# Kernel tuning notes

Measured on AMD Instinct MI355X. Metric: run time of the kernel, lower is better.

## Reference

```python
import jax, jax.numpy as jnp
import numpy as np

B, N, C, H = 8, 4096, 768, 8
EPS = 1e-12  # F.normalize eps


def setup_inputs() -> dict:
    key = jax.random.key(0)
    k1, k2, k3, k4 = jax.random.split(key, 4)
    x = jax.random.normal(k1, (B, N, C), dtype=jnp.float32)
    Wqkv = jax.random.normal(k2, (C, 3 * C), dtype=jnp.float32) * (1.0 / np.sqrt(C))
    temperature = jnp.ones((H, 1, 1), dtype=jnp.float32)
    Wproj = jax.random.normal(k3, (C, C), dtype=jnp.float32) * (1.0 / np.sqrt(C))
    bproj = jax.random.normal(k4, (C,), dtype=jnp.float32) * 0.01
    return {"x": x, "Wqkv": Wqkv, "temperature": temperature, "Wproj": Wproj, "bproj": bproj}


def _l2norm(t):
    # F.normalize(dim=-1): t / max(||t||_2, eps)
    n = jnp.sqrt(jnp.sum(t * t, axis=-1, keepdims=True))
    return t / jnp.maximum(n, EPS)


def reference(x, Wqkv, temperature, Wproj, bproj):
    b, n, c = x.shape
    h = temperature.shape[0]
    hd = c // h
    qkv = x @ Wqkv  # [B, N, 3C]
    qkv = qkv.reshape(b, n, 3, h, hd).transpose(2, 0, 3, 4, 1)  # [3, B, H, hd, N]
    q, k, v = qkv[0], qkv[1], qkv[2]
    q = _l2norm(q)  # normalize over token dim N
    k = _l2norm(k)
    # channel-channel attention: [B, H, hd, hd]
    attn = jnp.einsum('bhdn,bhen->bhde', q, k) * temperature  # temperature [H,1,1] broadcasts
    attn = jax.nn.softmax(attn, axis=-1)
    out = jnp.einsum('bhde,bhen->bhdn', attn, v)  # [B, H, hd, N]
    out = out.transpose(0, 3, 1, 2).reshape(b, n, c)  # [B, N, C]
    return out @ Wproj + bproj
```

## Files before the change

### kernel.cpp

```cpp
#include <hip/hip_runtime.h>
#include <stdint.h>


typedef __attribute__((ext_vector_type(8))) __bf16 bf16x8;
typedef __attribute__((ext_vector_type(4))) float f32x4;

__device__ __forceinline__ unsigned short f2b(float f) {
  uint32_t u = __float_as_uint(f);
  u += 0x7FFF + ((u >> 16) & 1);
  return (unsigned short)(u >> 16);
}

__device__ __forceinline__ void gload16(const void* g, void* l) {
  __builtin_amdgcn_global_load_lds(
      (__attribute__((address_space(1))) void*)(uintptr_t)g,
      (__attribute__((address_space(3))) void*)(uintptr_t)l, 16, 0, 0);
}

__device__ __forceinline__ float dot8(const unsigned short* a, const unsigned short* b) {
  uint4 va = *(const uint4*)a, vb = *(const uint4*)b;
  const unsigned short* pa = (const unsigned short*)&va;
  const unsigned short* pb = (const unsigned short*)&vb;
  float s = 0.f;
#pragma unroll
  for (int i = 0; i < 8; i++)
    s += __uint_as_float((uint32_t)pa[i] << 16) * __uint_as_float((uint32_t)pb[i] << 16);
  return s;
}

__global__ void cvt_x(const float* __restrict__ in, unsigned short* __restrict__ xb,
                      unsigned short* __restrict__ xbT) {
  __shared__ float tile[32][33];
  int bx = blockIdx.x, by = blockIdx.y, b = blockIdx.z;
  int tx = threadIdx.x & 31, ty = threadIdx.x >> 5;
  const float* src = in + (size_t)b * 4096 * 768;
  for (int r = ty; r < 32; r += 8) {
    float v = src[(size_t)(by * 32 + r) * 768 + bx * 32 + tx];
    tile[r][tx] = v;
    xb[((size_t)b * 4096 + by * 32 + r) * 768 + bx * 32 + tx] = f2b(v);
  }
  __syncthreads();
  for (int r = ty; r < 32; r += 8)
    xbT[((size_t)b * 768 + bx * 32 + r) * 4096 + by * 32 + tx] = f2b(tile[tx][r]);
}

__global__ void cvt_transpose(const float* __restrict__ in, unsigned short* __restrict__ out,
                              int K, int NC) {
  __shared__ float tile[32][33];
  int bx = blockIdx.x, by = blockIdx.y;
  int tx = threadIdx.x & 31, ty = threadIdx.x >> 5;
  for (int r = ty; r < 32; r += 8)
    tile[r][tx] = in[(size_t)(by * 32 + r) * NC + bx * 32 + tx];
  __syncthreads();
  for (int r = ty; r < 32; r += 8)
    out[(size_t)(bx * 32 + r) * K + by * 32 + tx] = f2b(tile[tx][r]);
}

#define BARX() asm volatile("s_barrier" ::: "memory")
#define WAITV(N) asm volatile("s_waitcnt vmcnt(" #N ")" ::: "memory")
#define SCHED() __builtin_amdgcn_sched_barrier(0)

#define STAGE(gbase, p, isB, h, t) do {                                             \
  unsigned short* _lb = &lds[(p)*32768 + (isB)*16384 + (h)*8192 + wid*1024];        \
  const unsigned short* _gb = (gbase) + (size_t)((h)*128 + wid*16)*768 + (t)*64 + lanegoff; \
  gload16(_gb, _lb);                                                                \
  gload16(_gb + 8*768, _lb + 512);                                                  \
} while (0)

#define LOAD_A(p, mh) do {                                                          \
  const unsigned short* _ab = &lds[(p)*32768 + (mh)*8192];                          \
  _Pragma("unroll") for (int _mi = 0; _mi < 4; _mi++)                               \
    _Pragma("unroll") for (int _kk = 0; _kk < 2; _kk++)                             \
      af[_mi][_kk] = *(const bf16x8*)&_ab[(wm*64 + _mi*16 + l16)*64 + ((_kk*4+quad)^(l16&7))*8]; \
} while (0)

#define LOAD_B(dst, p, nh) do {                                                     \
  const unsigned short* _bb = &lds[(p)*32768 + 16384 + (nh)*8192];                  \
  _Pragma("unroll") for (int _ni = 0; _ni < 2; _ni++)                               \
    _Pragma("unroll") for (int _kk = 0; _kk < 2; _kk++)                             \
      dst[_ni][_kk] = *(const bf16x8*)&_bb[(wn*32 + _ni*16 + l16)*64 + ((_kk*4+quad)^(l16&7))*8]; \
} while (0)

#define MFMA_PH(mh, nh, bfx) do {                                                   \
  __builtin_amdgcn_s_setprio(1);                                                    \
  _Pragma("unroll") for (int _m = 0; _m < 4; _m++)                                  \
    _Pragma("unroll") for (int _n = 0; _n < 2; _n++)                                \
      _Pragma("unroll") for (int _k = 0; _k < 2; _k++)                              \
        acc[(mh)*4+_m][(nh)*2+_n] = __builtin_amdgcn_mfma_f32_16x16x32_bf16(        \
            af[_m][_k], bfx[_n][_k], acc[(mh)*4+_m][(nh)*2+_n], 0, 0, 0);           \
  __builtin_amdgcn_s_setprio(0);                                                    \
} while (0)

__global__ __launch_bounds__(512, 2) void gemm_v(
    const unsigned short* __restrict__ A, const unsigned short* __restrict__ Bt,
    unsigned short* __restrict__ vT) {
  __shared__ __align__(16) unsigned short lds[65536];
  int lin = blockIdx.y * 3 + blockIdx.x;
  int swz = (lin & 7) * 48 + (lin >> 3);
  int bm = swz / 3;
  int bj = 6 + (swz - bm * 3);
  int m0 = bm * 256, j0 = bj * 256;
  int tid = threadIdx.x;
  int wid = tid >> 6, lane = tid & 63;
  int wm = wid >> 2, wn = wid & 3;
  int quad = lane >> 4, l16 = lane & 15;
  int srow = lane >> 3, sch = lane & 7;
  int cmem = sch ^ srow;
  int lanegoff = srow * 768 + cmem * 8;

  f32x4 acc[8][4];
  f32x4 z = {0.f, 0.f, 0.f, 0.f};
#pragma unroll
  for (int i = 0; i < 8; i++)
#pragma unroll
    for (int j = 0; j < 4; j++) acc[i][j] = z;

  bf16x8 af[4][2], bf0[2][2], bf1[2][2];

  const unsigned short* Ab2 = A + (size_t)m0 * 768;
  const unsigned short* Bb2 = Bt + (size_t)j0 * 768;

  STAGE(Ab2, 0, 0, 0, 0); STAGE(Bb2, 0, 1, 0, 0); STAGE(Bb2, 0, 1, 1, 0); STAGE(Ab2, 0, 0, 1, 0);
  STAGE(Ab2, 1, 0, 0, 1); STAGE(Bb2, 1, 1, 0, 1); STAGE(Bb2, 1, 1, 1, 1);
  WAITV(10);
  BARX();
  LOAD_A(0, 0);
  LOAD_B(bf0, 0, 0);
  WAITV(8);
  BARX();

  for (int t = 0; t < 10; t++) {
    int p = t & 1;
    LOAD_B(bf1, p, 1);
    STAGE(Ab2, p ^ 1, 0, 1, t + 1);
    BARX(); SCHED();
    MFMA_PH(0, 0, bf0);
    SCHED(); WAITV(8); BARX();
    STAGE(Ab2, p, 0, 0, t + 2);
    BARX(); SCHED();
    MFMA_PH(0, 1, bf1);
    SCHED();
    LOAD_A(p, 1);
    BARX();
    STAGE(Bb2, p, 1, 0, t + 2);
    BARX(); SCHED();
    MFMA_PH(1, 1, bf1);
    SCHED(); WAITV(8); BARX();
    STAGE(Bb2, p, 1, 1, t + 2);
    BARX(); SCHED();
    MFMA_PH(1, 0, bf0);
    SCHED();
    LOAD_A(p ^ 1, 0);
    LOAD_B(bf0, p ^ 1, 0);
    WAITV(8); BARX();
  }
  LOAD_B(bf1, 0, 1);
  STAGE(Ab2, 1, 0, 1, 11);
  BARX(); SCHED(); MFMA_PH(0, 0, bf0); SCHED(); WAITV(8); BARX();
  BARX(); SCHED(); MFMA_PH(0, 1, bf1); SCHED(); LOAD_A(0, 1); BARX();
  BARX(); SCHED(); MFMA_PH(1, 1, bf1); SCHED(); WAITV(4); BARX();
  BARX(); SCHED(); MFMA_PH(1, 0, bf0); SCHED(); LOAD_A(1, 0); LOAD_B(bf0, 1, 0); WAITV(2); BARX();
  LOAD_B(bf1, 1, 1);
  BARX(); SCHED(); MFMA_PH(0, 0, bf0); SCHED(); WAITV(0); BARX();
  BARX(); SCHED(); MFMA_PH(0, 1, bf1); SCHED(); LOAD_A(1, 1); BARX();
  BARX(); SCHED(); MFMA_PH(1, 1, bf1); SCHED(); BARX();
  BARX(); SCHED(); MFMA_PH(1, 0, bf0); SCHED(); BARX();

  int b = m0 >> 12;
  int n0 = m0 & 4095;
  int j0v = j0 - 1536;
#pragma unroll
  for (int mh = 0; mh < 2; mh++) {
    __syncthreads();
#pragma unroll
    for (int ml = 0; ml < 4; ml++) {
      int mi = mh * 4 + ml;
      int mloc = wm * 64 + ml * 16 + quad * 4;
#pragma unroll
      for (int ni = 0; ni < 4; ni++) {
        int jc = (ni >> 1) * 128 + wn * 32 + (ni & 1) * 16 + l16;
#pragma unroll
        for (int r = 0; r < 4; r++) lds[(mloc + r) * 264 + jc] = f2b(acc[mi][ni][r]);
      }
    }
    __syncthreads();
#pragma unroll
    for (int it = 0; it < 8; it++) {
      int id = it * 512 + tid;
      int mr = id >> 5, ch = id & 31;
      int cp = j0v + ch * 8;
      int hh = cp / 96, e = cp - hh * 96;
      size_t off = ((size_t)(b * 8 + hh) * 4096 + (n0 + mh * 128 + mr)) * 96 + e;
      *(uint4*)&vT[off] = *(const uint4*)&lds[mr * 264 + ch * 8];
    }
  }
}

__global__ __launch_bounds__(256, 2) void gemm_g(
    const unsigned short* __restrict__ xbT, unsigned short* __restrict__ G) {
  __shared__ __align__(16) unsigned short lds[16384];
  int bj = blockIdx.x;
  int bz = blockIdx.y;
  int b = bz / 6, mt = bz - b * 6;
  int m0 = mt * 128, j0 = bj * 128;
  int tid = threadIdx.x;
  int wid = tid >> 6, lane = tid & 63;
  int wm = wid >> 1, wn = wid & 1;
  int quad = lane >> 4, l16 = lane & 15;
  int srow = lane >> 3, sch = lane & 7;
  int cmem = sch ^ srow;

  f32x4 acc[4][4];
  f32x4 z = {0.f, 0.f, 0.f, 0.f};
#pragma unroll
  for (int i = 0; i < 4; i++)
#pragma unroll
    for (int j = 0; j < 4; j++) acc[i][j] = z;

  const unsigned short* Ab = xbT + ((size_t)b * 768 + m0) * 4096;
  const unsigned short* Bb = xbT + ((size_t)b * 768 + j0) * 4096;

  for (int k0 = 0; k0 < 4096; k0 += 64) {
#pragma unroll
    for (int i = 0; i < 4; i++) {
      int ig = wid * 4 + i;
      int row = ig * 8 + srow;
      gload16(Ab + (size_t)row * 4096 + k0 + cmem * 8, &lds[ig * 512]);
      gload16(Bb + (size_t)row * 4096 + k0 + cmem * 8, &lds[8192 + ig * 512]);
    }
    __syncthreads();
#pragma unroll
    for (int kk = 0; kk < 2; kk++) {
      int cs = ((kk * 4 + quad) ^ (l16 & 7)) * 8;
      bf16x8 af[4], bfr[4];
#pragma unroll
      for (int mi = 0; mi < 4; mi++)
        af[mi] = *(const bf16x8*)&lds[(wm * 64 + mi * 16 + l16) * 64 + cs];
#pragma unroll
      for (int ni = 0; ni < 4; ni++)
        bfr[ni] = *(const bf16x8*)&lds[8192 + (wn * 64 + ni * 16 + l16) * 64 + cs];
#pragma unroll
      for (int mi = 0; mi < 4; mi++)
#pragma unroll
        for (int ni = 0; ni < 4; ni++)
          acc[mi][ni] = __builtin_amdgcn_mfma_f32_16x16x32_bf16(af[mi], bfr[ni], acc[mi][ni], 0, 0, 0);
    }
    __syncthreads();
  }
  unsigned short* Gb = G + ((size_t)b * 768 + m0) * 768 + j0;
#pragma unroll
  for (int ni = 0; ni < 4; ni++)
#pragma unroll
    for (int mi = 0; mi < 4; mi++)
#pragma unroll
      for (int r = 0; r < 4; r++)
        Gb[(size_t)(wm * 64 + mi * 16 + quad * 4 + r) * 768 + wn * 64 + ni * 16 + l16] =
            f2b(acc[mi][ni][r]);
}

__global__ __launch_bounds__(256, 2) void gemm_t12(
    const unsigned short* __restrict__ G, const unsigned short* __restrict__ WqkvT,
    unsigned short* __restrict__ T12t) {
  __shared__ __align__(16) unsigned short lds[17408];
  int bj = blockIdx.x;
  int bz = blockIdx.y;
  int b = bz / 6, mt = bz - b * 6;
  int m0 = mt * 128, j0 = bj * 128;
  int tid = threadIdx.x;
  int wid = tid >> 6, lane = tid & 63;
  int wm = wid >> 1, wn = wid & 1;
  int quad = lane >> 4, l16 = lane & 15;
  int srow = lane >> 3, sch = lane & 7;
  int cmem = sch ^ srow;

  f32x4 acc[4][4];
  f32x4 z = {0.f, 0.f, 0.f, 0.f};
#pragma unroll
  for (int i = 0; i < 4; i++)
#pragma unroll
    for (int j = 0; j < 4; j++) acc[i][j] = z;

  const unsigned short* Ab = G + ((size_t)b * 768 + m0) * 768;
  const unsigned short* Bb = WqkvT + (size_t)j0 * 768;

  for (int k0 = 0; k0 < 768; k0 += 64) {
#pragma unroll
    for (int i = 0; i < 4; i++) {
      int ig = wid * 4 + i;
      int row = ig * 8 + srow;
      gload16(Ab + (size_t)row * 768 + k0 + cmem * 8, &lds[ig * 512]);
      gload16(Bb + (size_t)row * 768 + k0 + cmem * 8, &lds[8192 + ig * 512]);
    }
    __syncthreads();
#pragma unroll
    for (int kk = 0; kk < 2; kk++) {
      int cs = ((kk * 4 + quad) ^ (l16 & 7)) * 8;
      bf16x8 af[4], bfr[4];
#pragma unroll
      for (int mi = 0; mi < 4; mi++)
        af[mi] = *(const bf16x8*)&lds[(wm * 64 + mi * 16 + l16) * 64 + cs];
#pragma unroll
      for (int ni = 0; ni < 4; ni++)
        bfr[ni] = *(const bf16x8*)&lds[8192 + (wn * 64 + ni * 16 + l16) * 64 + cs];
#pragma unroll
      for (int mi = 0; mi < 4; mi++)
#pragma unroll
        for (int ni = 0; ni < 4; ni++)
          acc[mi][ni] = __builtin_amdgcn_mfma_f32_16x16x32_bf16(af[mi], bfr[ni], acc[mi][ni], 0, 0, 0);
    }
    __syncthreads();
  }
#pragma unroll
  for (int mi = 0; mi < 4; mi++)
#pragma unroll
    for (int ni = 0; ni < 4; ni++)
#pragma unroll
      for (int r = 0; r < 4; r++) {
        int m = wm * 64 + mi * 16 + quad * 4 + r;
        int cc = wn * 64 + ni * 16 + l16;
        lds[cc * 136 + m] = f2b(acc[mi][ni][r]);
      }
  __syncthreads();
#pragma unroll
  for (int it = 0; it < 8; it++) {
    int id = tid + it * 256;
    int jr = id >> 4, mc = id & 15;
    *(uint4*)&T12t[((size_t)b * 1536 + j0 + jr) * 768 + m0 + mc * 8] =
        *(const uint4*)&lds[jr * 136 + mc * 8];
  }
}

__global__ __launch_bounds__(256, 2) void softmax_s(
    const unsigned short* __restrict__ T12t, const unsigned short* __restrict__ WqkvT,
    const float* __restrict__ temp, unsigned short* __restrict__ attnB) {
  __shared__ __align__(16) unsigned short lds[24960];
  float* nq = (float*)&lds[24576];
  float* nk = (float*)&lds[24768];
  int bh = blockIdx.x;
  int b = bh >> 3, h = bh & 7;
  int tid = threadIdx.x, wid = tid >> 6, lane = tid & 63;
  int wm = wid >> 1, wn = wid & 1, quad = lane >> 4, l16 = lane & 15;
  int srow = lane >> 3, sch = lane & 7, cmem = sch ^ srow;

  const unsigned short* pb0 = T12t + ((size_t)b * 1536 + h * 96) * 768;
  const unsigned short* pb1 = WqkvT + (size_t)(h * 96) * 768;
  const unsigned short* pb2 = T12t + ((size_t)b * 1536 + 768 + h * 96) * 768;
  const unsigned short* pb3 = WqkvT + (size_t)(768 + h * 96) * 768;

  f32x4 acc[3][3];
  f32x4 z = {0.f, 0.f, 0.f, 0.f};
#pragma unroll
  for (int i = 0; i < 3; i++)
#pragma unroll
    for (int j = 0; j < 3; j++) acc[i][j] = z;
  float aq[3] = {0.f, 0.f, 0.f}, ak[3] = {0.f, 0.f, 0.f};

  for (int k0 = 0; k0 < 768; k0 += 64) {
#pragma unroll
    for (int i = 0; i < 3; i++) {
      int igrp = wid * 3 + i;
      int row = igrp * 8 + srow;
      size_t off = (size_t)row * 768 + k0 + cmem * 8;
      gload16(pb0 + off, &lds[igrp * 512]);
      gload16(pb1 + off, &lds[6144 + igrp * 512]);
      gload16(pb2 + off, &lds[12288 + igrp * 512]);
      gload16(pb3 + off, &lds[18432 + igrp * 512]);
    }
    __syncthreads();
#pragma unroll
    for (int kk = 0; kk < 2; kk++) {
      int cs = ((kk * 4 + quad) ^ (l16 & 7)) * 8;
      bf16x8 af[3], bfr[3];
#pragma unroll
      for (int mi = 0; mi < 3; mi++)
        af[mi] = *(const bf16x8*)&lds[(wm * 48 + mi * 16 + l16) * 64 + cs];
#pragma unroll
      for (int ni = 0; ni < 3; ni++)
        bfr[ni] = *(const bf16x8*)&lds[18432 + (wn * 48 + ni * 16 + l16) * 64 + cs];
#pragma unroll
      for (int mi = 0; mi < 3; mi++)
#pragma unroll
        for (int ni = 0; ni < 3; ni++)
          acc[mi][ni] = __builtin_amdgcn_mfma_f32_16x16x32_bf16(af[mi], bfr[ni], acc[mi][ni], 0, 0, 0);
    }
#pragma unroll
    for (int s = 0; s < 3; s++) {
      int idx = s * 256 + tid;
      int r = idx >> 3, ch = idx & 7;
      aq[s] += dot8(&lds[r * 64 + ch * 8], &lds[6144 + r * 64 + ch * 8]);
      ak[s] += dot8(&lds[12288 + r * 64 + ch * 8], &lds[18432 + r * 64 + ch * 8]);
    }
    __syncthreads();
  }
#pragma unroll
  for (int s = 0; s < 3; s++) {
    float vq = aq[s], vk = ak[s];
    vq += __shfl_down(vq, 4, 8); vq += __shfl_down(vq, 2, 8); vq += __shfl_down(vq, 1, 8);
    vk += __shfl_down(vk, 4, 8); vk += __shfl_down(vk, 2, 8); vk += __shfl_down(vk, 1, 8);
    if ((tid & 7) == 0) { nq[s * 32 + (tid >> 3)] = vq; nk[s * 32 + (tid >> 3)] = vk; }
  }
  __syncthreads();
  float* Sf = (float*)lds;
#pragma unroll
  for (int mi = 0; mi < 3; mi++)
#pragma unroll
    for (int ni = 0; ni < 3; ni++)
#pragma unroll
      for (int r = 0; r < 4; r++)
        Sf[(wm * 48 + mi * 16 + quad * 4 + r) * 97 + wn * 48 + ni * 16 + l16] = acc[mi][ni][r];
  if (tid < 96) nk[tid] = 1.0f / fmaxf(sqrtf(nk[tid]), 1e-12f);
  __syncthreads();
  float tval = temp[h];
  for (int r = wid; r < 96; r += 4) {
    float iq = tval / fmaxf(sqrtf(nq[r]), 1e-12f);
    float v0 = Sf[r * 97 + lane] * iq * nk[lane];
    float v1 = (lane < 32) ? Sf[r * 97 + 64 + lane] * iq * nk[64 + lane] : -1e30f;
    float mx = fmaxf(v0, v1);
#pragma unroll
    for (int off = 32; off; off >>= 1) mx = fmaxf(mx, __shfl_xor(mx, off, 64));
    float e0 = __expf(v0 - mx);
    float e1 = (lane < 32) ? __expf(v1 - mx) : 0.f;
    float sm = e0 + e1;
#pragma unroll
    for (int off = 32; off; off >>= 1) sm += __shfl_xor(sm, off, 64);
    float inv = 1.0f / sm;
    unsigned short* row = attnB + (size_t)bh * 9984 + r * 104;
    row[lane] = f2b(e0 * inv);
    if (lane < 32) row[64 + lane] = f2b(e1 * inv);
    else if (64 + lane < 104) row[64 + lane] = 0;
  }
}

__global__ __launch_bounds__(256, 4) void attn_v(
    const unsigned short* __restrict__ attnB, const unsigned short* __restrict__ vT,
    unsigned short* __restrict__ U) {
  __shared__ __align__(16) unsigned short lds[23552];
  int blk = blockIdx.x;
  int bh = blk >> 5, nc = blk & 31;
  int b = bh >> 3, h = bh & 7;
  int n0 = nc * 128;
  int tid = threadIdx.x, wid = tid >> 6, lane = tid & 63;
  int wm = wid >> 1, wn = wid & 1, quad = lane >> 4, l16 = lane & 15;

  const unsigned short* ab = attnB + (size_t)bh * 9984;
#pragma unroll
  for (int i = 0; i < 5; i++) {
    int id = i * 256 + tid;
    int ids = id < 1248 ? id : 1247;
    gload16(ab + (size_t)ids * 8, &lds[(i * 4 + wid) * 512]);
  }

  const unsigned short* vb = vT + (size_t)bh * 4096 * 96 + (size_t)n0 * 96;
#pragma unroll
  for (int i = 0; i < 7; i++) {
    int ig = wid + i * 4;
    if (ig < 26) {
      int id = ig * 64 + lane;
      int row = id / 13;
      int ch = id - row * 13;
      if (ch > 11) ch = 11;
      gload16(vb + (size_t)row * 96 + ch * 8, &lds[10240 + ig * 512]);
    }
  }
  __syncthreads();

  f32x4 acc[3][4];
  f32x4 z = {0.f, 0.f, 0.f, 0.f};
#pragma unroll
  for (int i = 0; i < 3; i++)
#pragma unroll
    for (int j = 0; j < 4; j++) acc[i][j] = z;
#pragma unroll
  for (int et = 0; et < 3; et++) {
    bf16x8 af[3], bfr[4];
#pragma unroll
    for (int mi = 0; mi < 3; mi++)
      af[mi] = *(const bf16x8*)&lds[(wm * 48 + mi * 16 + l16) * 104 + (et * 4 + quad) * 8];
#pragma unroll
    for (int ni = 0; ni < 4; ni++)
      bfr[ni] = *(const bf16x8*)&lds[10240 + (wn * 64 + ni * 16 + l16) * 104 + (et * 4 + quad) * 8];
#pragma unroll
    for (int mi = 0; mi < 3; mi++)
#pragma unroll
      for (int ni = 0; ni < 4; ni++)
        acc[mi][ni] = __builtin_amdgcn_mfma_f32_16x16x32_bf16(af[mi], bfr[ni], acc[mi][ni], 0, 0, 0);
  }
  __syncthreads();

#pragma unroll
  for (int mi = 0; mi < 3; mi++)
#pragma unroll
    for (int ni = 0; ni < 4; ni++)
#pragma unroll
      for (int r = 0; r < 4; r++) {
        int d = wm * 48 + mi * 16 + quad * 4 + r;
        int n = wn * 64 + ni * 16 + l16;
        lds[n * 104 + d] = f2b(acc[mi][ni][r]);
      }
  __syncthreads();
#pragma unroll
  for (int it = 0; it < 6; it++) {
    int id = tid + it * 256;
    int nr = id / 12, ch = id - nr * 12;
    *(uint4*)&U[((size_t)(b * 4096 + n0 + nr)) * 768 + h * 96 + ch * 8] =
        *(const uint4*)&lds[nr * 104 + ch * 8];
  }
}

__global__ __launch_bounds__(256, 2) void gemm_out(
    const unsigned short* __restrict__ A, const unsigned short* __restrict__ Bt,
    const float* __restrict__ bias, float* __restrict__ out) {
  __shared__ __align__(16) unsigned short lds[16384];
  int bj = blockIdx.x;
  int bm = blockIdx.y;
  int m0 = bm * 128, j0 = bj * 128;
  int tid = threadIdx.x;
  int wid = tid >> 6, lane = tid & 63;
  int wm = wid >> 1, wn = wid & 1;
  int quad = lane >> 4, l16 = lane & 15;
  int srow = lane >> 3, sch = lane & 7;
  int cmem = sch ^ srow;

  f32x4 acc[4][4];
  f32x4 z = {0.f, 0.f, 0.f, 0.f};
#pragma unroll
  for (int i = 0; i < 4; i++)
#pragma unroll
    for (int j = 0; j < 4; j++) acc[i][j] = z;

  const unsigned short* Ab = A + (size_t)m0 * 768;
  const unsigned short* Bb = Bt + (size_t)j0 * 768;

  for (int k0 = 0; k0 < 768; k0 += 64) {
#pragma unroll
    for (int i = 0; i < 4; i++) {
      int ig = wid * 4 + i;
      int row = ig * 8 + srow;
      gload16(Ab + (size_t)row * 768 + k0 + cmem * 8, &lds[ig * 512]);
      gload16(Bb + (size_t)row * 768 + k0 + cmem * 8, &lds[8192 + ig * 512]);
    }
    __syncthreads();
#pragma unroll
    for (int kk = 0; kk < 2; kk++) {
      int cs = ((kk * 4 + quad) ^ (l16 & 7)) * 8;
      bf16x8 af[4], bfr[4];
#pragma unroll
      for (int mi = 0; mi < 4; mi++)
        af[mi] = *(const bf16x8*)&lds[(wm * 64 + mi * 16 + l16) * 64 + cs];
#pragma unroll
      for (int ni = 0; ni < 4; ni++)
        bfr[ni] = *(const bf16x8*)&lds[8192 + (wn * 64 + ni * 16 + l16) * 64 + cs];
#pragma unroll
      for (int mi = 0; mi < 4; mi++)
#pragma unroll
        for (int ni = 0; ni < 4; ni++)
          acc[mi][ni] = __builtin_amdgcn_mfma_f32_16x16x32_bf16(af[mi], bfr[ni], acc[mi][ni], 0, 0, 0);
    }
    __syncthreads();
  }
#pragma unroll
  for (int ni = 0; ni < 4; ni++) {
    int ccol = j0 + wn * 64 + ni * 16 + l16;
    float bv = bias[ccol];
#pragma unroll
    for (int mi = 0; mi < 4; mi++)
#pragma unroll
      for (int r = 0; r < 4; r++)
        out[(size_t)(m0 + wm * 64 + mi * 16 + quad * 4 + r) * 768 + ccol] = acc[mi][ni][r] + bv;
  }
}

extern "C" void kernel_launch(void* const* d_in, const int* in_sizes, int n_in,
                              void* d_out, int out_size, void* d_ws, size_t ws_size,
                              hipStream_t stream) {
  const float* x = (const float*)d_in[0];
  const float* Wqkv = (const float*)d_in[1];
  const float* temp = (const float*)d_in[2];
  const float* Wproj = (const float*)d_in[3];
  const float* bproj = (const float*)d_in[4];
  float* out = (float*)d_out;
  char* ws = (char*)d_ws;

  unsigned short* xb     = (unsigned short*)(ws);
  unsigned short* WqkvT  = (unsigned short*)(ws + 50331648);
  unsigned short* WprojT = (unsigned short*)(ws + 53870592);
  unsigned short* xbT    = (unsigned short*)(ws + 55050240);
  unsigned short* vT     = (unsigned short*)(ws + 105381888);
  unsigned short* U      = (unsigned short*)(ws + 155713536);
  unsigned short* G      = (unsigned short*)(ws + 206045184);
  unsigned short* T12t   = (unsigned short*)(ws + 215482368);
  unsigned short* attnB  = (unsigned short*)(ws + 234356736);

  cvt_x<<<dim3(24, 128, 8), dim3(256), 0, stream>>>(x, xb, xbT);
  cvt_transpose<<<dim3(72, 24), dim3(256), 0, stream>>>(Wqkv, WqkvT, 768, 2304);
  cvt_transpose<<<dim3(24, 24), dim3(256), 0, stream>>>(Wproj, WprojT, 768, 768);
  gemm_g<<<dim3(6, 48), dim3(256), 0, stream>>>(xbT, G);
  gemm_t12<<<dim3(12, 48), dim3(256), 0, stream>>>(G, WqkvT, T12t);
  softmax_s<<<dim3(64), dim3(256), 0, stream>>>(T12t, WqkvT, temp, attnB);
  gemm_v<<<dim3(3, 128), dim3(512), 0, stream>>>(xb, WqkvT, vT);
  attn_v<<<dim3(2048), dim3(256), 0, stream>>>(attnB, vT, U);
  gemm_out<<<dim3(6, 256), dim3(256), 0, stream>>>(U, WprojT, bproj, out);
}
```

Baseline: 464.7 us.

## Exploit Gram symmetry, merge G and V GEMMs, vectorize conversion kernels

Computes only the lower-triangular tiles of the per-batch Gram matrix x^T x and mirrors off-diagonal tiles through LDS, cutting redundant MFMA work. The G and V projection GEMMs are merged into a single launch so their blocks share the GPU. The x conversion is vectorized with 64x64 tiles, and the two weight transposes are combined into one kernel. The V GEMM now uses the simpler 128x128 non-pipelined loop instead of the hand-scheduled 256x256 kernel, which may lower its efficiency.

Measured after the change: 415.4 us. 10.6% less time.

```diff
diff --git a/kernel.cpp b/kernel.cpp
--- a/kernel.cpp
+++ b/kernel.cpp
@@ -28,181 +28,63 @@
   return s;
 }
 
-__global__ void cvt_x(const float* __restrict__ in, unsigned short* __restrict__ xb,
-                      unsigned short* __restrict__ xbT) {
+__global__ __launch_bounds__(256) void cvt_x(const float* __restrict__ in,
+                                             unsigned short* __restrict__ xb,
+                                             unsigned short* __restrict__ xbT) {
+  __shared__ unsigned short tileT[64][66];
+  int c0 = blockIdx.x * 64, n0 = blockIdx.y * 64, b = blockIdx.z;
+  int tid = threadIdx.x;
+  int col4 = tid & 15, rbase = tid >> 4;
+  const float* src = in + (size_t)b * 4096 * 768;
+#pragma unroll
+  for (int rr = 0; rr < 4; rr++) {
+    int r = rr * 16 + rbase;
+    float4 v = *(const float4*)&src[(size_t)(n0 + r) * 768 + c0 + col4 * 4];
+    ushort4 o;
+    o.x = f2b(v.x); o.y = f2b(v.y); o.z = f2b(v.z); o.w = f2b(v.w);
+    *(ushort4*)&xb[((size_t)b * 4096 + n0 + r) * 768 + c0 + col4 * 4] = o;
+    tileT[col4 * 4 + 0][r] = o.x;
+    tileT[col4 * 4 + 1][r] = o.y;
+    tileT[col4 * 4 + 2][r] = o.z;
+    tileT[col4 * 4 + 3][r] = o.w;
+  }
+  __syncthreads();
+#pragma unroll
+  for (int rr = 0; rr < 4; rr++) {
+    int cc = rr * 16 + rbase;
+    ushort4 w;
+    w.x = tileT[cc][col4 * 4 + 0];
+    w.y = tileT[cc][col4 * 4 + 1];
+    w.z = tileT[cc][col4 * 4 + 2];
+    w.w = tileT[cc][col4 * 4 + 3];
+    *(ushort4*)&xbT[((size_t)b * 768 + c0 + cc) * 4096 + n0 + col4 * 4] = w;
+  }
+}
+
+__global__ __launch_bounds__(256) void cvt_w(const float* __restrict__ Wqkv,
+                                             const float* __restrict__ Wproj,
+                                             unsigned short* __restrict__ WqkvT,
+                                             unsigned short* __restrict__ WprojT) {
   __shared__ float tile[32][33];
-  int bx = blockIdx.x, by = blockIdx.y, b = blockIdx.z;
-  int tx = threadIdx.x & 31, ty = threadIdx.x >> 5;
-  const float* src = in + (size_t)b * 4096 * 768;
-  for (int r = ty; r < 32; r += 8) {
-    float v = src[(size_t)(by * 32 + r) * 768 + bx * 32 + tx];
-    tile[r][tx] = v;
-    xb[((size_t)b * 4096 + by * 32 + r) * 768 + bx * 32 + tx] = f2b(v);
-  }
-  __syncthreads();
-  for (int r = ty; r < 32; r += 8)
-    xbT[((size_t)b * 768 + bx * 32 + r) * 4096 + by * 32 + tx] = f2b(tile[tx][r]);
-}
-
-__global__ void cvt_transpose(const float* __restrict__ in, unsigned short* __restrict__ out,
-                              int K, int NC) {
-  __shared__ float tile[32][33];
+  int z = blockIdx.z;
+  const float* in = z ? Wproj : Wqkv;
+  unsigned short* out = z ? WprojT : WqkvT;
+  int NC = z ? 768 : 2304;
+  if (z && blockIdx.x >= 24) return;
   int bx = blockIdx.x, by = blockIdx.y;
   int tx = threadIdx.x & 31, ty = threadIdx.x >> 5;
   for (int r = ty; r < 32; r += 8)
     tile[r][tx] = in[(size_t)(by * 32 + r) * NC + bx * 32 + tx];
   __syncthreads();
   for (int r = ty; r < 32; r += 8)
-    out[(size_t)(bx * 32 + r) * K + by * 32 + tx] = f2b(tile[tx][r]);
-}
-
-#define BARX() asm volatile("s_barrier" ::: "memory")
-#define WAITV(N) asm volatile("s_waitcnt vmcnt(" #N ")" ::: "memory")
-#define SCHED() __builtin_amdgcn_sched_barrier(0)
-
-#define STAGE(gbase, p, isB, h, t) do {                                             \
-  unsigned short* _lb = &lds[(p)*32768 + (isB)*16384 + (h)*8192 + wid*1024];        \
-  const unsigned short* _gb = (gbase) + (size_t)((h)*128 + wid*16)*768 + (t)*64 + lanegoff; \
-  gload16(_gb, _lb);                                                                \
-  gload16(_gb + 8*768, _lb + 512);                                                  \
-} while (0)
-
-#define LOAD_A(p, mh) do {                                                          \
-  const unsigned short* _ab = &lds[(p)*32768 + (mh)*8192];                          \
-  _Pragma("unroll") for (int _mi = 0; _mi < 4; _mi++)                               \
-    _Pragma("unroll") for (int _kk = 0; _kk < 2; _kk++)                             \
-      af[_mi][_kk] = *(const bf16x8*)&_ab[(wm*64 + _mi*16 + l16)*64 + ((_kk*4+quad)^(l16&7))*8]; \
-} while (0)
-
-#define LOAD_B(dst, p, nh) do {                                                     \
-  const unsigned short* _bb = &lds[(p)*32768 + 16384 + (nh)*8192];                  \
-  _Pragma("unroll") for (int _ni = 0; _ni < 2; _ni++)                               \
-    _Pragma("unroll") for (int _kk = 0; _kk < 2; _kk++)                             \
-      dst[_ni][_kk] = *(const bf16x8*)&_bb[(wn*32 + _ni*16 + l16)*64 + ((_kk*4+quad)^(l16&7))*8]; \
-} while (0)
-
-#define MFMA_PH(mh, nh, bfx) do {                                                   \
-  __builtin_amdgcn_s_setprio(1);                                                    \
-  _Pragma("unroll") for (int _m = 0; _m < 4; _m++)                                  \
-    _Pragma("unroll") for (int _n = 0; _n < 2; _n++)                                \
-      _Pragma("unroll") for (int _k = 0; _k < 2; _k++)                              \
-        acc[(mh)*4+_m][(nh)*2+_n] = __builtin_amdgcn_mfma_f32_16x16x32_bf16(        \
-            af[_m][_k], bfx[_n][_k], acc[(mh)*4+_m][(nh)*2+_n], 0, 0, 0);           \
-  __builtin_amdgcn_s_setprio(0);                                                    \
-} while (0)
-
-__global__ __launch_bounds__(512, 2) void gemm_v(
-    const unsigned short* __restrict__ A, const unsigned short* __restrict__ Bt,
+    out[(size_t)(bx * 32 + r) * 768 + by * 32 + tx] = f2b(tile[tx][r]);
+}
+
+__global__ __launch_bounds__(256, 2) void gemm_gv(
+    const unsigned short* __restrict__ xbT, const unsigned short* __restrict__ xb,
+    const unsigned short* __restrict__ WqkvT, unsigned short* __restrict__ G,
     unsigned short* __restrict__ vT) {
-  __shared__ __align__(16) unsigned short lds[65536];
-  int lin = blockIdx.y * 3 + blockIdx.x;
-  int swz = (lin & 7) * 48 + (lin >> 3);
-  int bm = swz / 3;
-  int bj = 6 + (swz - bm * 3);
-  int m0 = bm * 256, j0 = bj * 256;
-  int tid = threadIdx.x;
-  int wid = tid >> 6, lane = tid & 63;
-  int wm = wid >> 2, wn = wid & 3;
-  int quad = lane >> 4, l16 = lane & 15;
-  int srow = lane >> 3, sch = lane & 7;
-  int cmem = sch ^ srow;
-  int lanegoff = srow * 768 + cmem * 8;
-
-  f32x4 acc[8][4];
-  f32x4 z = {0.f, 0.f, 0.f, 0.f};
-#pragma unroll
-  for (int i = 0; i < 8; i++)
-#pragma unroll
-    for (int j = 0; j < 4; j++) acc[i][j] = z;
-
-  bf16x8 af[4][2], bf0[2][2], bf1[2][2];
-
-  const unsigned short* Ab2 = A + (size_t)m0 * 768;
-  const unsigned short* Bb2 = Bt + (size_t)j0 * 768;
-
-  STAGE(Ab2, 0, 0, 0, 0); STAGE(Bb2, 0, 1, 0, 0); STAGE(Bb2, 0, 1, 1, 0); STAGE(Ab2, 0, 0, 1, 0);
-  STAGE(Ab2, 1, 0, 0, 1); STAGE(Bb2, 1, 1, 0, 1); STAGE(Bb2, 1, 1, 1, 1);
-  WAITV(10);
-  BARX();
-  LOAD_A(0, 0);
-  LOAD_B(bf0, 0, 0);
-  WAITV(8);
-  BARX();
-
-  for (int t = 0; t < 10; t++) {
-    int p = t & 1;
-    LOAD_B(bf1, p, 1);
-    STAGE(Ab2, p ^ 1, 0, 1, t + 1);
-    BARX(); SCHED();
-    MFMA_PH(0, 0, bf0);
-    SCHED(); WAITV(8); BARX();
-    STAGE(Ab2, p, 0, 0, t + 2);
-    BARX(); SCHED();
-    MFMA_PH(0, 1, bf1);
-    SCHED();
-    LOAD_A(p, 1);
-    BARX();
-    STAGE(Bb2, p, 1, 0, t + 2);
-    BARX(); SCHED();
-    MFMA_PH(1, 1, bf1);
-    SCHED(); WAITV(8); BARX();
-    STAGE(Bb2, p, 1, 1, t + 2);
-    BARX(); SCHED();
-    MFMA_PH(1, 0, bf0);
-    SCHED();
-    LOAD_A(p ^ 1, 0);
-    LOAD_B(bf0, p ^ 1, 0);
-    WAITV(8); BARX();
-  }
-  LOAD_B(bf1, 0, 1);
-  STAGE(Ab2, 1, 0, 1, 11);
-  BARX(); SCHED(); MFMA_PH(0, 0, bf0); SCHED(); WAITV(8); BARX();
-  BARX(); SCHED(); MFMA_PH(0, 1, bf1); SCHED(); LOAD_A(0, 1); BARX();
-  BARX(); SCHED(); MFMA_PH(1, 1, bf1); SCHED(); WAITV(4); BARX();
-  BARX(); SCHED(); MFMA_PH(1, 0, bf0); SCHED(); LOAD_A(1, 0); LOAD_B(bf0, 1, 0); WAITV(2); BARX();
-  LOAD_B(bf1, 1, 1);
-  BARX(); SCHED(); MFMA_PH(0, 0, bf0); SCHED(); WAITV(0); BARX();
-  BARX(); SCHED(); MFMA_PH(0, 1, bf1); SCHED(); LOAD_A(1, 1); BARX();
-  BARX(); SCHED(); MFMA_PH(1, 1, bf1); SCHED(); BARX();
-  BARX(); SCHED(); MFMA_PH(1, 0, bf0); SCHED(); BARX();
-
-  int b = m0 >> 12;
-  int n0 = m0 & 4095;
-  int j0v = j0 - 1536;
-#pragma unroll
-  for (int mh = 0; mh < 2; mh++) {
-    __syncthreads();
-#pragma unroll
-    for (int ml = 0; ml < 4; ml++) {
-      int mi = mh * 4 + ml;
-      int mloc = wm * 64 + ml * 16 + quad * 4;
-#pragma unroll
-      for (int ni = 0; ni < 4; ni++) {
-        int jc = (ni >> 1) * 128 + wn * 32 + (ni & 1) * 16 + l16;
-#pragma unroll
-        for (int r = 0; r < 4; r++) lds[(mloc + r) * 264 + jc] = f2b(acc[mi][ni][r]);
-      }
-    }
-    __syncthreads();
-#pragma unroll
-    for (int it = 0; it < 8; it++) {
-      int id = it * 512 + tid;
-      int mr = id >> 5, ch = id & 31;
-      int cp = j0v + ch * 8;
-      int hh = cp / 96, e = cp - hh * 96;
-      size_t off = ((size_t)(b * 8 + hh) * 4096 + (n0 + mh * 128 + mr)) * 96 + e;
-      *(uint4*)&vT[off] = *(const uint4*)&lds[mr * 264 + ch * 8];
-    }
-  }
-}
-
-__global__ __launch_bounds__(256, 2) void gemm_g(
-    const unsigned short* __restrict__ xbT, unsigned short* __restrict__ G) {
-  __shared__ __align__(16) unsigned short lds[16384];
-  int bj = blockIdx.x;
-  int bz = blockIdx.y;
-  int b = bz / 6, mt = bz - b * 6;
-  int m0 = mt * 128, j0 = bj * 128;
+  __shared__ __align__(16) unsigned short lds[17408];
   int tid = threadIdx.x;
   int wid = tid >> 6, lane = tid & 63;
   int wm = wid >> 1, wn = wid & 1;
@@ -217,45 +99,131 @@
 #pragma unroll
     for (int j = 0; j < 4; j++) acc[i][j] = z;
 
-  const unsigned short* Ab = xbT + ((size_t)b * 768 + m0) * 4096;
-  const unsigned short* Bb = xbT + ((size_t)b * 768 + j0) * 4096;
-
-  for (int k0 = 0; k0 < 4096; k0 += 64) {
-#pragma unroll
-    for (int i = 0; i < 4; i++) {
-      int ig = wid * 4 + i;
-      int row = ig * 8 + srow;
-      gload16(Ab + (size_t)row * 4096 + k0 + cmem * 8, &lds[ig * 512]);
-      gload16(Bb + (size_t)row * 4096 + k0 + cmem * 8, &lds[8192 + ig * 512]);
-    }
-    __syncthreads();
-#pragma unroll
-    for (int kk = 0; kk < 2; kk++) {
-      int cs = ((kk * 4 + quad) ^ (l16 & 7)) * 8;
-      bf16x8 af[4], bfr[4];
+  if (blockIdx.x < 168) {
+    int lin = blockIdx.x;
+    int widx = (lin & 7) * 21 + (lin >> 3);
+    int b = widx / 21, ti = widx - b * 21;
+    int mt = 0;
+    while ((mt + 1) * (mt + 2) / 2 <= ti) mt++;
+    int jt = ti - mt * (mt + 1) / 2;
+    int m0 = mt * 128, j0 = jt * 128;
+    const unsigned short* Ab = xbT + ((size_t)b * 768 + m0) * 4096;
+    const unsigned short* Bb = xbT + ((size_t)b * 768 + j0) * 4096;
+
+    for (int k0 = 0; k0 < 4096; k0 += 64) {
+#pragma unroll
+      for (int i = 0; i < 4; i++) {
+        int ig = wid * 4 + i;
+        int row = ig * 8 + srow;
+        gload16(Ab + (size_t)row * 4096 + k0 + cmem * 8, &lds[ig * 512]);
+        gload16(Bb + (size_t)row * 4096 + k0 + cmem * 8, &lds[8192 + ig * 512]);
+      }
+      __syncthreads();
+#pragma unroll
+      for (int kk = 0; kk < 2; kk++) {
+        int cs = ((kk * 4 + quad) ^ (l16 & 7)) * 8;
+        bf16x8 af[4], bfr[4];
+#pragma unroll
+        for (int mi = 0; mi < 4; mi++)
+          af[mi] = *(const bf16x8*)&lds[(wm * 64 + mi * 16 + l16) * 64 + cs];
+#pragma unroll
+        for (int ni = 0; ni < 4; ni++)
+          bfr[ni] = *(const bf16x8*)&lds[8192 + (wn * 64 + ni * 16 + l16) * 64 + cs];
+#pragma unroll
+        for (int mi = 0; mi < 4; mi++)
+#pragma unroll
+          for (int ni = 0; ni < 4; ni++)
+            acc[mi][ni] = __builtin_amdgcn_mfma_f32_16x16x32_bf16(af[mi], bfr[ni], acc[mi][ni], 0, 0, 0);
+      }
+      __syncthreads();
+    }
+    unsigned short* Gb = G + ((size_t)b * 768 + m0) * 768 + j0;
+#pragma unroll
+    for (int ni = 0; ni < 4; ni++)
 #pragma unroll
       for (int mi = 0; mi < 4; mi++)
-        af[mi] = *(const bf16x8*)&lds[(wm * 64 + mi * 16 + l16) * 64 + cs];
+#pragma unroll
+        for (int r = 0; r < 4; r++)
+          Gb[(size_t)(wm * 64 + mi * 16 + quad * 4 + r) * 768 + wn * 64 + ni * 16 + l16] =
+              f2b(acc[mi][ni][r]);
+    if (mt != jt) {
+      __syncthreads();
+#pragma unroll
+      for (int mi = 0; mi < 4; mi++)
+#pragma unroll
+        for (int ni = 0; ni < 4; ni++)
+#pragma unroll
+          for (int r = 0; r < 4; r++) {
+            int m = wm * 64 + mi * 16 + quad * 4 + r;
+            int cc = wn * 64 + ni * 16 + l16;
+            lds[cc * 136 + m] = f2b(acc[mi][ni][r]);
+          }
+      __syncthreads();
+#pragma unroll
+      for (int it = 0; it < 8; it++) {
+        int id = tid + it * 256;
+        int jr = id >> 4, mc = id & 15;
+        *(uint4*)&G[((size_t)b * 768 + j0 + jr) * 768 + m0 + mc * 8] =
+            *(const uint4*)&lds[jr * 136 + mc * 8];
+      }
+    }
+  } else {
+    int lin2 = blockIdx.x - 168;
+    int bm = lin2 / 6, jt = lin2 - bm * 6;
+    int m0 = bm * 128, j0 = jt * 128;
+    const unsigned short* Ab = xb + (size_t)m0 * 768;
+    const unsigned short* Bb = WqkvT + (size_t)(1536 + j0) * 768;
+
+    for (int k0 = 0; k0 < 768; k0 += 64) {
+#pragma unroll
+      for (int i = 0; i < 4; i++) {
+        int ig = wid * 4 + i;
+        int row = ig * 8 + srow;
+        gload16(Ab + (size_t)row * 768 + k0 + cmem * 8, &lds[ig * 512]);
+        gload16(Bb + (size_t)row * 768 + k0 + cmem * 8, &lds[8192 + ig * 512]);
+      }
+      __syncthreads();
+#pragma unroll
+      for (int kk = 0; kk < 2; kk++) {
+        int cs = ((kk * 4 + quad) ^ (l16 & 7)) * 8;
+        bf16x8 af[4], bfr[4];
+#pragma unroll
+        for (int mi = 0; mi < 4; mi++)
+          af[mi] = *(const bf16x8*)&lds[(wm * 64 + mi * 16 + l16) * 64 + cs];
+#pragma unroll
+        for (int ni = 0; ni < 4; ni++)
+          bfr[ni] = *(const bf16x8*)&lds[8192 + (wn * 64 + ni * 16 + l16) * 64 + cs];
+#pragma unroll
+        for (int mi = 0; mi < 4; mi++)
+#pragma unroll
+          for (int ni = 0; ni < 4; ni++)
+            acc[mi][ni] = __builtin_amdgcn_mfma_f32_16x16x32_bf16(af[mi], bfr[ni], acc[mi][ni], 0, 0, 0);
+      }
+      __syncthreads();
+    }
+    int b = m0 >> 12;
+    int n0 = m0 & 4095;
+#pragma unroll
+    for (int mi = 0; mi < 4; mi++)
 #pragma unroll
       for (int ni = 0; ni < 4; ni++)
-        bfr[ni] = *(const bf16x8*)&lds[8192 + (wn * 64 + ni * 16 + l16) * 64 + cs];
-#pragma unroll
-      for (int mi = 0; mi < 4; mi++)
-#pragma unroll
-        for (int ni = 0; ni < 4; ni++)
-          acc[mi][ni] = __builtin_amdgcn_mfma_f32_16x16x32_bf16(af[mi], bfr[ni], acc[mi][ni], 0, 0, 0);
-    }
-    __syncthreads();
-  }
-  unsigned short* Gb = G + ((size_t)b * 768 + m0) * 768 + j0;
-#pragma unroll
-  for (int ni = 0; ni < 4; ni++)
-#pragma unroll
-    for (int mi = 0; mi < 4; mi++)
-#pragma unroll
-      for (int r = 0; r < 4; r++)
-        Gb[(size_t)(wm * 64 + mi * 16 + quad * 4 + r) * 768 + wn * 64 + ni * 16 + l16] =
-            f2b(acc[mi][ni][r]);
+#pragma unroll
+        for (int r = 0; r < 4; r++) {
+          int m = wm * 64 + mi * 16 + quad * 4 + r;
+          int cc = wn * 64 + ni * 16 + l16;
+          lds[m * 136 + cc] = f2b(acc[mi][ni][r]);
+        }
+    __syncthreads();
+#pragma unroll
+    for (int it = 0; it < 8; it++) {
+      int id = tid + it * 256;
+      int mr = id >> 4, ch = id & 15;
+      int cp = j0 + ch * 8;
+      int hh = cp / 96, e = cp - hh * 96;
+      size_t off = ((size_t)(b * 8 + hh) * 4096 + (n0 + mr)) * 96 + e;
+      *(uint4*)&vT[off] = *(const uint4*)&lds[mr * 136 + ch * 8];
+    }
+  }
 }
 
 __global__ __launch_bounds__(256, 2) void gemm_t12(
@@ -591,13 +559,11 @@
   unsigned short* T12t   = (unsigned short*)(ws + 215482368);
   unsigned short* attnB  = (unsigned short*)(ws + 234356736);
 
-  cvt_x<<<dim3(24, 128, 8), dim3(256), 0, stream>>>(x, xb, xbT);
-  cvt_transpose<<<dim3(72, 24), dim3(256), 0, stream>>>(Wqkv, WqkvT, 768, 2304);
-  cvt_transpose<<<dim3(24, 24), dim3(256), 0, stream>>>(Wproj, WprojT, 768, 768);
-  gemm_g<<<dim3(6, 48), dim3(256), 0, stream>>>(xbT, G);
+  cvt_x<<<dim3(12, 64, 8), dim3(256), 0, stream>>>(x, xb, xbT);
+  cvt_w<<<dim3(72, 24, 2), dim3(256), 0, stream>>>(Wqkv, Wproj, WqkvT, WprojT);
+  gemm_gv<<<dim3(1704), dim3(256), 0, stream>>>(xbT, xb, WqkvT, G, vT);
   gemm_t12<<<dim3(12, 48), dim3(256), 0, stream>>>(G, WqkvT, T12t);
   softmax_s<<<dim3(64), dim3(256), 0, stream>>>(T12t, WqkvT, temp, attnB);
-  gemm_v<<<dim3(3, 128), dim3(512), 0, stream>>>(xb, WqkvT, vT);
   attn_v<<<dim3(2048), dim3(256), 0, stream>>>(attnB, vT, U);
   gemm_out<<<dim3(6, 256), dim3(256), 0, stream>>>(U, WprojT, bproj, out);
 }
```
